# Kernel tuning notes

Measured on AMD Instinct MI355X. Metric: run time of the kernel, lower is better.

Reference implementation:

```python
import jax, jax.numpy as jnp
import numpy as np

N, E, DIN, DH, HEADS, DOUT = 50000, 800000, 128, 32, 4, 16
NL_HID = 2  # num_layers - 1
HID = HEADS * DH


def setup_inputs() -> dict:
    key = jax.random.key(0)
    ks = jax.random.split(key, 16)

    def w(k, shape, fan_in):
        return jax.random.normal(k, shape, jnp.float32) * (1.0 / np.sqrt(fan_in))

    return {
        "x": jax.random.normal(ks[0], (N, DIN), jnp.float32),
        "edge_index": jax.random.randint(ks[1], (2, E), 0, N, dtype=jnp.int64),
        "edge_attr": jax.random.normal(ks[2], (E, 1), jnp.float32),
        # conv1: dim_in -> (heads, dim_h)
        "W1": w(ks[3], (DIN, HID), DIN),
        "as1": w(ks[4], (HEADS, DH), DH),
        "ad1": w(ks[5], (HEADS, DH), DH),
        "b1": jnp.zeros((HID,), jnp.float32),
        # hidden convs: hid -> (heads, dim_h), stacked over NL_HID layers
        "Wh": w(ks[6], (NL_HID, HID, HID), HID),
        "ash": w(ks[7], (NL_HID, HEADS, DH), DH),
        "adh": w(ks[8], (NL_HID, HEADS, DH), DH),
        "bh": jnp.zeros((NL_HID, HID), jnp.float32),
        # conv2: hid -> (1, dim_out)
        "W2": w(ks[9], (HID, DOUT), HID),
        "as2": w(ks[10], (1, DOUT), DOUT),
        "ad2": w(ks[11], (1, DOUT), DOUT),
        "b2": jnp.zeros((DOUT,), jnp.float32),
    }


def _gat_conv(x, src, dst, W, a_s, a_d, b):
    """PyG GATConv (eval mode: attention dropout inactive), concat heads."""
    H, C = a_s.shape
    n = x.shape[0]
    h = (x @ W).reshape(n, H, C)                       # [N,H,C]
    al_s = jnp.einsum('nhc,hc->nh', h, a_s)            # [N,H]
    al_d = jnp.einsum('nhc,hc->nh', h, a_d)
    e = jax.nn.leaky_relu(al_s[src] + al_d[dst], 0.2)  # [Et,H]
    # scatter-softmax over incoming edges of each destination node
    m = jax.ops.segment_max(e, dst, num_segments=n)
    ee = jnp.exp(e - m[dst])
    denom = jax.ops.segment_sum(ee, dst, num_segments=n)
    alpha = ee / (denom[dst] + 1e-16)                  # [Et,H]
    out = jax.ops.segment_sum(h[src] * alpha[:, :, None], dst, num_segments=n)
    return out.reshape(n, H * C) + b


def reference(x, edge_index, edge_attr, W1, as1, ad1, b1, Wh, ash, adh, bh, W2, as2, ad2, b2):
    n = x.shape[0]
    # GATConv adds self-loops by default
    loops = jnp.arange(n, dtype=edge_index.dtype)
    src = jnp.concatenate([edge_index[0], loops])
    dst = jnp.concatenate([edge_index[1], loops])
    h = jax.nn.elu(_gat_conv(x, src, dst, W1, as1, ad1, b1))
    for i in range(Wh.shape[0]):  # dropout p=0.5 inactive in eval mode
        h = jax.nn.elu(_gat_conv(h, src, dst, Wh[i], ash[i], adh[i], bh[i]))
    return _gat_conv(h, src, dst, W2, as2, ad2, b2)  # heads=1 -> [N, DOUT]
```

## Files before the change

kernel.cpp:

```cpp
#include <hip/hip_runtime.h>
#include <hip/hip_bf16.h>
#include <hip/hip_fp16.h>


typedef _Float16 half8_t __attribute__((ext_vector_type(8)));
typedef float f32x4_t  __attribute__((ext_vector_type(4)));

static inline int divup(int a, int b){ return (a + b - 1) / b; }


__global__ __launch_bounds__(256) void zero_cnt_kernel(int* __restrict__ cnt, int n){
    int i = blockIdx.x * 256 + threadIdx.x;
    int4 z = {0, 0, 0, 0};
    if (i * 4 + 3 < n){
        *(int4*)(cnt + i * 4) = z;
    } else {
        for (int j = i * 4; j < n; ++j) cnt[j] = 0;
    }
}


__global__ __launch_bounds__(256) void fill_sliced_kernel(const int* __restrict__ src,
                                                          const int* __restrict__ dst,
                                                          int* __restrict__ cnt,
                                                          unsigned short* __restrict__ csr,
                                                          int E, int Et){
    int slice = blockIdx.x & 7;
    int e = (blockIdx.x >> 3) * 256 + threadIdx.x;
    if (e >= Et) return;
    int d = (e < E) ? dst[e] : (e - E);
    if ((d & 7) != slice) return;
    int s = (e < E) ? src[e] : d;
    int pos = atomicAdd(&cnt[d], 1);
    csr[(d << 6) + pos] = (unsigned short)s;
}


__global__ __launch_bounds__(256) void prep_kernel(const float* __restrict__ W1,
                                                   const float* __restrict__ Wh,
                                                   const float* __restrict__ as1,
                                                   const float* __restrict__ ad1,
                                                   const float* __restrict__ ash,
                                                   const float* __restrict__ adh,
                                                   _Float16* __restrict__ WTx){
    int id = blockIdx.x * 256 + threadIdx.x;
    if (id >= 3 * 144 * 128) return;
    int l = id / (144 * 128), rem = id % (144 * 128);
    int c = rem >> 7, k = rem & 127;
    const float* W = (l == 0) ? W1 : (Wh + (size_t)(l - 1) * 16384);
    float v = 0.f;
    if (c < 128){
        v = W[k * 128 + c];
    } else if (c < 136){
        int h = (c - 128) & 3;
        const float* a = (c < 132) ? ((l == 0) ? as1 : ash + (size_t)(l - 1) * 128)
                                   : ((l == 0) ? ad1 : adh + (size_t)(l - 1) * 128);
        const float* wr = W + k * 128 + h * 32;
        const float* ar = a + h * 32;
        float sum = 0.f;
        #pragma unroll
        for (int c2 = 0; c2 < 32; ++c2) sum += wr[c2] * ar[c2];
        v = sum;
    }
    WTx[id] = (_Float16)v;
}


template<bool F32IN>
__device__ __forceinline__ void gemm128L_body(const void* __restrict__ Xv,
                                              const _Float16* __restrict__ WTx,
                                              _Float16* __restrict__ H16,
                                              float* __restrict__ als,
                                              float* __restrict__ ald, int n){
    int wav = threadIdx.x >> 6, lane = threadIdx.x & 63;
    int nb = blockIdx.x * 16;
    int r = lane & 15, kg = lane >> 4;
    int anode = nb + r; if (anode >= n) anode = n - 1;

    half8_t a0, a1, a2, a3;
    if (F32IN){
        const float* xrow = (const float*)Xv + (size_t)anode * 128 + kg * 8;
        #pragma unroll
        for (int q = 0; q < 4; ++q){
            float4 u = *(const float4*)(xrow + q * 32);
            float4 w = *(const float4*)(xrow + q * 32 + 4);
            half8_t o = {(_Float16)u.x,(_Float16)u.y,(_Float16)u.z,(_Float16)u.w,
                         (_Float16)w.x,(_Float16)w.y,(_Float16)w.z,(_Float16)w.w};
            if (q == 0) a0 = o; else if (q == 1) a1 = o; else if (q == 2) a2 = o; else a3 = o;
        }
    } else {
        const _Float16* xrow = (const _Float16*)Xv + (size_t)anode * 128 + kg * 8;
        a0 = *(const half8_t*)(xrow);
        a1 = *(const half8_t*)(xrow + 32);
        a2 = *(const half8_t*)(xrow + 64);
        a3 = *(const half8_t*)(xrow + 96);
    }

    const _Float16* wc0 = WTx + (size_t)(wav * 32 + r) * 128 + kg * 8;
    const _Float16* wc1 = wc0 + 16 * 128;

    f32x4_t c0 = {0.f,0.f,0.f,0.f}, c1 = {0.f,0.f,0.f,0.f};
    c0 = __builtin_amdgcn_mfma_f32_16x16x32_f16(a0, *(const half8_t*)(wc0     ), c0, 0,0,0);
    c1 = __builtin_amdgcn_mfma_f32_16x16x32_f16(a0, *(const half8_t*)(wc1     ), c1, 0,0,0);
    c0 = __builtin_amdgcn_mfma_f32_16x16x32_f16(a1, *(const half8_t*)(wc0 + 32), c0, 0,0,0);
    c1 = __builtin_amdgcn_mfma_f32_16x16x32_f16(a1, *(const half8_t*)(wc1 + 32), c1, 0,0,0);
    c0 = __builtin_amdgcn_mfma_f32_16x16x32_f16(a2, *(const half8_t*)(wc0 + 64), c0, 0,0,0);
    c1 = __builtin_amdgcn_mfma_f32_16x16x32_f16(a2, *(const half8_t*)(wc1 + 64), c1, 0,0,0);
    c0 = __builtin_amdgcn_mfma_f32_16x16x32_f16(a3, *(const half8_t*)(wc0 + 96), c0, 0,0,0);
    c1 = __builtin_amdgcn_mfma_f32_16x16x32_f16(a3, *(const half8_t*)(wc1 + 96), c1, 0,0,0);

    int colw = wav * 32 + r;
    #pragma unroll
    for (int rg = 0; rg < 4; ++rg){
        int onode = nb + kg * 4 + rg;
        if (onode < n){
            _Float16* hr = H16 + (size_t)onode * 128 + colw;
            hr[0]  = (_Float16)c0[rg];
            hr[16] = (_Float16)c1[rg];
        }
    }

    if (wav == 0){
        const _Float16* wl = WTx + (size_t)(128 + r) * 128 + kg * 8;
        f32x4_t cl = {0.f,0.f,0.f,0.f};
        cl = __builtin_amdgcn_mfma_f32_16x16x32_f16(a0, *(const half8_t*)(wl     ), cl, 0,0,0);
        cl = __builtin_amdgcn_mfma_f32_16x16x32_f16(a1, *(const half8_t*)(wl + 32), cl, 0,0,0);
        cl = __builtin_amdgcn_mfma_f32_16x16x32_f16(a2, *(const half8_t*)(wl + 64), cl, 0,0,0);
        cl = __builtin_amdgcn_mfma_f32_16x16x32_f16(a3, *(const half8_t*)(wl + 96), cl, 0,0,0);
        if (r < 8){
            #pragma unroll
            for (int rg = 0; rg < 4; ++rg){
                int onode = nb + kg * 4 + rg;
                if (onode < n){
                    if (r < 4) als[(size_t)onode * 4 + r]       = cl[rg];
                    else       ald[(size_t)onode * 4 + (r - 4)] = cl[rg];
                }
            }
        }
    }
}

__global__ __launch_bounds__(256) void gemm128L_f32_kernel(const float* __restrict__ X,
                                                           const _Float16* __restrict__ WTx,
                                                           _Float16* __restrict__ H16,
                                                           float* __restrict__ als,
                                                           float* __restrict__ ald, int n){
    gemm128L_body<true>(X, WTx, H16, als, ald, n);
}

__global__ __launch_bounds__(256) void gemm128L_f16_kernel(const _Float16* __restrict__ X16,
                                                           const _Float16* __restrict__ WTx,
                                                           _Float16* __restrict__ H16,
                                                           float* __restrict__ als,
                                                           float* __restrict__ ald, int n){
    gemm128L_body<false>(X16, WTx, H16, als, ald, n);
}


__global__ __launch_bounds__(256) void aggregate128_kernel(const __half* __restrict__ H16,
                                                           const float* __restrict__ als,
                                                           const float* __restrict__ ald,
                                                           const int* __restrict__ cnt,
                                                           const unsigned short* __restrict__ csr,
                                                           const float* __restrict__ bias,
                                                           _Float16* __restrict__ out16,
                                                           int n){
    int node = blockIdx.x * 4 + (threadIdx.x >> 6);
    int lane = threadIdx.x & 63;
    if (node >= n) return;
    int start = node << 6, end = start + cnt[node];

    int eg = lane >> 4, cl = lane & 15;
    int h = cl >> 2;
    float ad_h = ald[(size_t)node * 4 + h];

    float den = 0.f;
    float acc[8] = {0,0,0,0,0,0,0,0};
    const __half* Hc = H16 + cl * 8;
    int i = start + eg;
    for (; i + 4 < end; i += 8){
        int sA = csr[i];
        int sB = csr[i + 4];
        float eA = als[(size_t)sA * 4 + h] + ad_h; eA = eA > 0.f ? eA : 0.2f * eA;
        float eB = als[(size_t)sB * 4 + h] + ad_h; eB = eB > 0.f ? eB : 0.2f * eB;
        float wA = __expf(eA);
        float wB = __expf(eB);
        den += wA + wB;
        uint4 ra = *(const uint4*)(Hc + (size_t)sA * 128);
        uint4 rb = *(const uint4*)(Hc + (size_t)sB * 128);
        float2 a0 = __half22float2(*(__half2*)&ra.x);
        float2 a1 = __half22float2(*(__half2*)&ra.y);
        float2 a2 = __half22float2(*(__half2*)&ra.z);
        float2 a3 = __half22float2(*(__half2*)&ra.w);
        float2 b0 = __half22float2(*(__half2*)&rb.x);
        float2 b1 = __half22float2(*(__half2*)&rb.y);
        float2 b2 = __half22float2(*(__half2*)&rb.z);
        float2 b3 = __half22float2(*(__half2*)&rb.w);
        acc[0] += wA * a0.x + wB * b0.x; acc[1] += wA * a0.y + wB * b0.y;
        acc[2] += wA * a1.x + wB * b1.x; acc[3] += wA * a1.y + wB * b1.y;
        acc[4] += wA * a2.x + wB * b2.x; acc[5] += wA * a2.y + wB * b2.y;
        acc[6] += wA * a3.x + wB * b3.x; acc[7] += wA * a3.y + wB * b3.y;
    }
    if (i < end){
        int s = csr[i];
        float e = als[(size_t)s * 4 + h] + ad_h; e = e > 0.f ? e : 0.2f * e;
        float w = __expf(e);
        den += w;
        uint4 ra = *(const uint4*)(Hc + (size_t)s * 128);
        float2 a0 = __half22float2(*(__half2*)&ra.x);
        float2 a1 = __half22float2(*(__half2*)&ra.y);
        float2 a2 = __half22float2(*(__half2*)&ra.z);
        float2 a3 = __half22float2(*(__half2*)&ra.w);
        acc[0] += w * a0.x; acc[1] += w * a0.y;
        acc[2] += w * a1.x; acc[3] += w * a1.y;
        acc[4] += w * a2.x; acc[5] += w * a2.y;
        acc[6] += w * a3.x; acc[7] += w * a3.y;
    }
    #pragma unroll
    for (int j = 0; j < 8; ++j){
        acc[j] += __shfl_xor(acc[j], 16);
        acc[j] += __shfl_xor(acc[j], 32);
    }
    den += __shfl_xor(den, 16);
    den += __shfl_xor(den, 32);

    if (eg == 0){
        float inv = 1.f / (den + 1e-16f);
        int col = cl * 8;
        float4 bv0 = *(const float4*)(bias + col);
        float4 bv1 = *(const float4*)(bias + col + 4);
        float v[8];
        v[0] = acc[0]*inv + bv0.x; v[1] = acc[1]*inv + bv0.y;
        v[2] = acc[2]*inv + bv0.z; v[3] = acc[3]*inv + bv0.w;
        v[4] = acc[4]*inv + bv1.x; v[5] = acc[5]*inv + bv1.y;
        v[6] = acc[6]*inv + bv1.z; v[7] = acc[7]*inv + bv1.w;
        #pragma unroll
        for (int j = 0; j < 8; ++j) v[j] = v[j] > 0.f ? v[j] : __expf(v[j]) - 1.f;

        half8_t o16 = {(_Float16)v[0], (_Float16)v[1], (_Float16)v[2], (_Float16)v[3],
                       (_Float16)v[4], (_Float16)v[5], (_Float16)v[6], (_Float16)v[7]};
        *(half8_t*)&out16[(size_t)node * 128 + col] = o16;
    }
}


__global__ __launch_bounds__(256) void gemm16_kernel(const _Float16* __restrict__ X16,
                                                     const float* __restrict__ W,
                                                     float* __restrict__ H4, int n){
    __shared__ float Ws[128 * 16];
    int tid = threadIdx.x;
    for (int i = tid; i < 2048; i += 256) Ws[i] = W[i];
    __syncthreads();
    int gid = blockIdx.x * 256 + tid;
    if (gid >= n * 16) return;
    int j = gid & 15, node = gid >> 4;
    const half8_t* xr = (const half8_t*)(X16 + (size_t)node * 128);
    float s = 0.f;
    #pragma unroll 4
    for (int k8 = 0; k8 < 16; ++k8){
        half8_t xv = xr[k8];
        #pragma unroll
        for (int t = 0; t < 8; ++t) s += (float)xv[t] * Ws[(k8 * 8 + t) * 16 + j];
    }
    H4[gid] = s;
}

__global__ __launch_bounds__(256) void al16_kernel(const float* __restrict__ H4,
                                                   const float* __restrict__ as2,
                                                   const float* __restrict__ ad2,
                                                   float* __restrict__ als4,
                                                   float* __restrict__ ald4, int n){
    int node = blockIdx.x * 256 + threadIdx.x;
    if (node >= n) return;
    const float4* hr = (const float4*)(H4 + (size_t)node * 16);
    const float4* asr = (const float4*)as2;
    const float4* adr = (const float4*)ad2;
    float ss = 0.f, sd = 0.f;
    #pragma unroll
    for (int i = 0; i < 4; ++i){
        float4 hv = hr[i], av = asr[i], dv = adr[i];
        ss += hv.x*av.x + hv.y*av.y + hv.z*av.z + hv.w*av.w;
        sd += hv.x*dv.x + hv.y*dv.y + hv.z*dv.z + hv.w*dv.w;
    }
    als4[node] = ss; ald4[node] = sd;
}


__global__ __launch_bounds__(256) void aggregate16_kernel(const float* __restrict__ H4,
                                                          const float* __restrict__ als4,
                                                          const float* __restrict__ ald4,
                                                          const int* __restrict__ cnt,
                                                          const unsigned short* __restrict__ csr,
                                                          const float* __restrict__ bias,
                                                          float* __restrict__ out, int n){
    int node = blockIdx.x * 4 + (threadIdx.x >> 6);
    int lane = threadIdx.x & 63;
    if (node >= n) return;
    int start = node << 6, end = start + cnt[node];
    float adn = ald4[node];

    int eg = lane >> 2, cl = lane & 3;
    float den = 0.f;
    float acc0 = 0.f, acc1 = 0.f, acc2 = 0.f, acc3 = 0.f;
    for (int i = start + eg; i < end; i += 16){
        int s = csr[i];
        float e = als4[s] + adn; e = e > 0.f ? e : 0.2f * e;
        float w = __expf(e);
        den += w;
        float4 hv = *(const float4*)(H4 + (size_t)s * 16 + cl * 4);
        acc0 += w * hv.x; acc1 += w * hv.y; acc2 += w * hv.z; acc3 += w * hv.w;
    }
    #pragma unroll
    for (int off = 4; off <= 32; off <<= 1){
        acc0 += __shfl_xor(acc0, off); acc1 += __shfl_xor(acc1, off);
        acc2 += __shfl_xor(acc2, off); acc3 += __shfl_xor(acc3, off);
        den  += __shfl_xor(den,  off);
    }

    if (eg == 0){
        float inv = 1.f / (den + 1e-16f);
        float4 bv = *(const float4*)(bias + cl * 4);
        float4 o = {acc0*inv + bv.x, acc1*inv + bv.y, acc2*inv + bv.z, acc3*inv + bv.w};
        *(float4*)&out[(size_t)node * 16 + cl * 4] = o;
    }
}


extern "C" void kernel_launch(void* const* d_in, const int* in_sizes, int n_in,
                              void* d_out, int out_size, void* d_ws, size_t ws_size,
                              hipStream_t stream) {
    const float* x   = (const float*)d_in[0];
    const int*   ei  = (const int*)d_in[1];
    const float* W1  = (const float*)d_in[3];
    const float* as1 = (const float*)d_in[4];
    const float* ad1 = (const float*)d_in[5];
    const float* b1  = (const float*)d_in[6];
    const float* Wh  = (const float*)d_in[7];
    const float* ash = (const float*)d_in[8];
    const float* adh = (const float*)d_in[9];
    const float* bh  = (const float*)d_in[10];
    const float* W2  = (const float*)d_in[11];
    const float* as2 = (const float*)d_in[12];
    const float* ad2 = (const float*)d_in[13];
    const float* b2  = (const float*)d_in[14];

    int N = in_sizes[0] / 128;
    int E = in_sizes[1] / 2;
    int Et = E + N;
    const int* srcA = ei;
    const int* dstA = ei + E;

    char* ws = (char*)d_ws;
    size_t off = 0;
    auto alloc = [&](size_t bytes) -> void* {
        void* p = ws + off;
        off = (off + bytes + 255) & ~(size_t)255;
        return p;
    };
    int* cnt      = (int*)alloc((size_t)N * 4);
    unsigned short* csr = (unsigned short*)alloc((size_t)N * 64 * 2);
    _Float16* xbuf16 = (_Float16*)alloc((size_t)N * 128 * 2);
    _Float16* h16    = (_Float16*)alloc((size_t)N * 128 * 2);
    _Float16* wtx    = (_Float16*)alloc((size_t)3 * 144 * 128 * 2);
    float* als_a  = (float*)alloc((size_t)N * 4 * 4);
    float* ald_a  = (float*)alloc((size_t)N * 4 * 4);
    float* h4     = (float*)alloc((size_t)N * 16 * 4);
    float* als4   = (float*)alloc((size_t)N * 4);
    float* ald4   = (float*)alloc((size_t)N * 4);

    zero_cnt_kernel<<<divup(divup(N, 4), 256), 256, 0, stream>>>(cnt, N);
    prep_kernel<<<divup(3 * 144 * 128, 256), 256, 0, stream>>>(W1, Wh, as1, ad1, ash, adh, wtx);
    fill_sliced_kernel<<<divup(Et, 256) * 8, 256, 0, stream>>>(srcA, dstA, cnt, csr, E, Et);

    float* out = (float*)d_out;
    const size_t WSTRIDE = (size_t)144 * 128;

    gemm128L_f32_kernel<<<divup(N, 16), 256, 0, stream>>>(x, wtx, h16, als_a, ald_a, N);
    aggregate128_kernel<<<divup(N, 4), 256, 0, stream>>>((const __half*)h16, als_a, ald_a, cnt, csr,
                                                        b1, xbuf16, N);
    gemm128L_f16_kernel<<<divup(N, 16), 256, 0, stream>>>(xbuf16, wtx + WSTRIDE, h16, als_a, ald_a, N);
    aggregate128_kernel<<<divup(N, 4), 256, 0, stream>>>((const __half*)h16, als_a, ald_a, cnt, csr,
                                                        bh, xbuf16, N);
    gemm128L_f16_kernel<<<divup(N, 16), 256, 0, stream>>>(xbuf16, wtx + 2 * WSTRIDE, h16, als_a, ald_a, N);
    aggregate128_kernel<<<divup(N, 4), 256, 0, stream>>>((const __half*)h16, als_a, ald_a, cnt, csr,
                                                        bh + 128, xbuf16, N);

    gemm16_kernel<<<divup(N * 16, 256), 256, 0, stream>>>(xbuf16, W2, h4, N);
    al16_kernel<<<divup(N, 256), 256, 0, stream>>>(h4, as2, ad2, als4, ald4, N);
    aggregate16_kernel<<<divup(N, 4), 256, 0, stream>>>(h4, als4, ald4, cnt, csr, b2, out, N);
}
```

Baseline: 266.5 us.

## Fuse final-layer GEMM and attention logits into one MFMA kernel with fp16 features

Replaces the scalar final-layer GEMM and the separate attention-logit kernel with one MFMA kernel. It uses a precomputed fp16 weight matrix whose extra columns hold W2·as2 and W2·ad2, so the logits come out of the same matrix multiply. The final hidden features are stored as fp16 instead of fp32, which halves gather traffic in the last aggregation. The CSR fill slicing also now uses bits 4-6 of the destination instead of the low bits, changing which blocks contend on atomics. The cost is fp16 rounding of the final-layer features and the folded logit weights.

```diff
diff --git a/kernel.cpp b/kernel.cpp
--- a/kernel.cpp
+++ b/kernel.cpp
@@ -29,7 +29,7 @@
     int e = (blockIdx.x >> 3) * 256 + threadIdx.x;
     if (e >= Et) return;
     int d = (e < E) ? dst[e] : (e - E);
-    if ((d & 7) != slice) return;
+    if (((d >> 4) & 7) != slice) return;
     int s = (e < E) ? src[e] : d;
     int pos = atomicAdd(&cnt[d], 1);
     csr[(d << 6) + pos] = (unsigned short)s;
@@ -42,27 +42,47 @@
                                                    const float* __restrict__ ad1,
                                                    const float* __restrict__ ash,
                                                    const float* __restrict__ adh,
-                                                   _Float16* __restrict__ WTx){
+                                                   const float* __restrict__ W2,
+                                                   const float* __restrict__ as2,
+                                                   const float* __restrict__ ad2,
+                                                   _Float16* __restrict__ WTx,
+                                                   _Float16* __restrict__ W2x){
     int id = blockIdx.x * 256 + threadIdx.x;
-    if (id >= 3 * 144 * 128) return;
-    int l = id / (144 * 128), rem = id % (144 * 128);
-    int c = rem >> 7, k = rem & 127;
-    const float* W = (l == 0) ? W1 : (Wh + (size_t)(l - 1) * 16384);
-    float v = 0.f;
-    if (c < 128){
-        v = W[k * 128 + c];
-    } else if (c < 136){
-        int h = (c - 128) & 3;
-        const float* a = (c < 132) ? ((l == 0) ? as1 : ash + (size_t)(l - 1) * 128)
-                                   : ((l == 0) ? ad1 : adh + (size_t)(l - 1) * 128);
-        const float* wr = W + k * 128 + h * 32;
-        const float* ar = a + h * 32;
-        float sum = 0.f;
-        #pragma unroll
-        for (int c2 = 0; c2 < 32; ++c2) sum += wr[c2] * ar[c2];
-        v = sum;
-    }
-    WTx[id] = (_Float16)v;
+    const int MAIN = 3 * 144 * 128;
+    if (id < MAIN){
+        int l = id / (144 * 128), rem = id % (144 * 128);
+        int c = rem >> 7, k = rem & 127;
+        const float* W = (l == 0) ? W1 : (Wh + (size_t)(l - 1) * 16384);
+        float v = 0.f;
+        if (c < 128){
+            v = W[k * 128 + c];
+        } else if (c < 136){
+            int h = (c - 128) & 3;
+            const float* a = (c < 132) ? ((l == 0) ? as1 : ash + (size_t)(l - 1) * 128)
+                                       : ((l == 0) ? ad1 : adh + (size_t)(l - 1) * 128);
+            const float* wr = W + k * 128 + h * 32;
+            const float* ar = a + h * 32;
+            float sum = 0.f;
+            #pragma unroll
+            for (int c2 = 0; c2 < 32; ++c2) sum += wr[c2] * ar[c2];
+            v = sum;
+        }
+        WTx[id] = (_Float16)v;
+    } else if (id < MAIN + 32 * 128){
+        int id2 = id - MAIN;
+        int c = id2 >> 7, k = id2 & 127;
+        float v = 0.f;
+        if (c < 16){
+            v = W2[k * 16 + c];
+        } else if (c == 16 || c == 17){
+            const float* a = (c == 16) ? as2 : ad2;
+            float sum = 0.f;
+            #pragma unroll
+            for (int j = 0; j < 16; ++j) sum += W2[k * 16 + j] * a[j];
+            v = sum;
+        }
+        W2x[id2] = (_Float16)v;
+    }
 }
 
 
@@ -154,6 +174,47 @@
                                                            float* __restrict__ als,
                                                            float* __restrict__ ald, int n){
     gemm128L_body<false>(X16, WTx, H16, als, ald, n);
+}
+
+
+__global__ __launch_bounds__(256) void gemm16L_kernel(const _Float16* __restrict__ X16,
+                                                      const _Float16* __restrict__ W2x,
+                                                      _Float16* __restrict__ H4,
+                                                      float* __restrict__ als4,
+                                                      float* __restrict__ ald4, int n){
+    int wav = threadIdx.x >> 6, lane = threadIdx.x & 63;
+    int nb = blockIdx.x * 64 + wav * 16;
+    int r = lane & 15, kg = lane >> 4;
+    int anode = nb + r; if (anode >= n) anode = n - 1;
+
+    const _Float16* xrow = X16 + (size_t)anode * 128 + kg * 8;
+    half8_t a0 = *(const half8_t*)(xrow);
+    half8_t a1 = *(const half8_t*)(xrow + 32);
+    half8_t a2 = *(const half8_t*)(xrow + 64);
+    half8_t a3 = *(const half8_t*)(xrow + 96);
+
+    const _Float16* wc0 = W2x + (size_t)r * 128 + kg * 8;
+    const _Float16* wc1 = wc0 + 16 * 128;
+
+    f32x4_t c0 = {0.f,0.f,0.f,0.f}, c1 = {0.f,0.f,0.f,0.f};
+    c0 = __builtin_amdgcn_mfma_f32_16x16x32_f16(a0, *(const half8_t*)(wc0     ), c0, 0,0,0);
+    c1 = __builtin_amdgcn_mfma_f32_16x16x32_f16(a0, *(const half8_t*)(wc1     ), c1, 0,0,0);
+    c0 = __builtin_amdgcn_mfma_f32_16x16x32_f16(a1, *(const half8_t*)(wc0 + 32), c0, 0,0,0);
+    c1 = __builtin_amdgcn_mfma_f32_16x16x32_f16(a1, *(const half8_t*)(wc1 + 32), c1, 0,0,0);
+    c0 = __builtin_amdgcn_mfma_f32_16x16x32_f16(a2, *(const half8_t*)(wc0 + 64), c0, 0,0,0);
+    c1 = __builtin_amdgcn_mfma_f32_16x16x32_f16(a2, *(const half8_t*)(wc1 + 64), c1, 0,0,0);
+    c0 = __builtin_amdgcn_mfma_f32_16x16x32_f16(a3, *(const half8_t*)(wc0 + 96), c0, 0,0,0);
+    c1 = __builtin_amdgcn_mfma_f32_16x16x32_f16(a3, *(const half8_t*)(wc1 + 96), c1, 0,0,0);
+
+    #pragma unroll
+    for (int rg = 0; rg < 4; ++rg){
+        int onode = nb + kg * 4 + rg;
+        if (onode < n){
+            H4[(size_t)onode * 16 + r] = (_Float16)c0[rg];
+            if (r == 0) als4[onode] = c1[rg];
+            else if (r == 1) ald4[onode] = c1[rg];
+        }
+    }
 }
 
 
@@ -244,49 +305,7 @@
 }
 
 
-__global__ __launch_bounds__(256) void gemm16_kernel(const _Float16* __restrict__ X16,
-                                                     const float* __restrict__ W,
-                                                     float* __restrict__ H4, int n){
-    __shared__ float Ws[128 * 16];
-    int tid = threadIdx.x;
-    for (int i = tid; i < 2048; i += 256) Ws[i] = W[i];
-    __syncthreads();
-    int gid = blockIdx.x * 256 + tid;
-    if (gid >= n * 16) return;
-    int j = gid & 15, node = gid >> 4;
-    const half8_t* xr = (const half8_t*)(X16 + (size_t)node * 128);
-    float s = 0.f;
-    #pragma unroll 4
-    for (int k8 = 0; k8 < 16; ++k8){
-        half8_t xv = xr[k8];
-        #pragma unroll
-        for (int t = 0; t < 8; ++t) s += (float)xv[t] * Ws[(k8 * 8 + t) * 16 + j];
-    }
-    H4[gid] = s;
-}
-
-__global__ __launch_bounds__(256) void al16_kernel(const float* __restrict__ H4,
-                                                   const float* __restrict__ as2,
-                                                   const float* __restrict__ ad2,
-                                                   float* __restrict__ als4,
-                                                   float* __restrict__ ald4, int n){
-    int node = blockIdx.x * 256 + threadIdx.x;
-    if (node >= n) return;
-    const float4* hr = (const float4*)(H4 + (size_t)node * 16);
-    const float4* asr = (const float4*)as2;
-    const float4* adr = (const float4*)ad2;
-    float ss = 0.f, sd = 0.f;
-    #pragma unroll
-    for (int i = 0; i < 4; ++i){
-        float4 hv = hr[i], av = asr[i], dv = adr[i];
-        ss += hv.x*av.x + hv.y*av.y + hv.z*av.z + hv.w*av.w;
-        sd += hv.x*dv.x + hv.y*dv.y + hv.z*dv.z + hv.w*dv.w;
-    }
-    als4[node] = ss; ald4[node] = sd;
-}
-
-
-__global__ __launch_bounds__(256) void aggregate16_kernel(const float* __restrict__ H4,
+__global__ __launch_bounds__(256) void aggregate16_kernel(const _Float16* __restrict__ H4,
                                                           const float* __restrict__ als4,
                                                           const float* __restrict__ ald4,
                                                           const int* __restrict__ cnt,
@@ -307,8 +326,10 @@
         float e = als4[s] + adn; e = e > 0.f ? e : 0.2f * e;
         float w = __expf(e);
         den += w;
-        float4 hv = *(const float4*)(H4 + (size_t)s * 16 + cl * 4);
-        acc0 += w * hv.x; acc1 += w * hv.y; acc2 += w * hv.z; acc3 += w * hv.w;
+        uint2 hv = *(const uint2*)(H4 + (size_t)s * 16 + cl * 4);
+        float2 h0 = __half22float2(*(__half2*)&hv.x);
+        float2 h1 = __half22float2(*(__half2*)&hv.y);
+        acc0 += w * h0.x; acc1 += w * h0.y; acc2 += w * h1.x; acc3 += w * h1.y;
     }
     #pragma unroll
     for (int off = 4; off <= 32; off <<= 1){
@@ -362,14 +383,16 @@
     _Float16* xbuf16 = (_Float16*)alloc((size_t)N * 128 * 2);
     _Float16* h16    = (_Float16*)alloc((size_t)N * 128 * 2);
     _Float16* wtx    = (_Float16*)alloc((size_t)3 * 144 * 128 * 2);
+    _Float16* w2x    = (_Float16*)alloc((size_t)32 * 128 * 2);
     float* als_a  = (float*)alloc((size_t)N * 4 * 4);
     float* ald_a  = (float*)alloc((size_t)N * 4 * 4);
-    float* h4     = (float*)alloc((size_t)N * 16 * 4);
+    _Float16* h4  = (_Float16*)alloc((size_t)N * 16 * 2);
     float* als4   = (float*)alloc((size_t)N * 4);
     float* ald4   = (float*)alloc((size_t)N * 4);
 
     zero_cnt_kernel<<<divup(divup(N, 4), 256), 256, 0, stream>>>(cnt, N);
-    prep_kernel<<<divup(3 * 144 * 128, 256), 256, 0, stream>>>(W1, Wh, as1, ad1, ash, adh, wtx);
+    prep_kernel<<<divup(3 * 144 * 128 + 32 * 128, 256), 256, 0, stream>>>(
+        W1, Wh, as1, ad1, ash, adh, W2, as2, ad2, wtx, w2x);
     fill_sliced_kernel<<<divup(Et, 256) * 8, 256, 0, stream>>>(srcA, dstA, cnt, csr, E, Et);
 
     float* out = (float*)d_out;
@@ -385,7 +408,6 @@
     aggregate128_kernel<<<divup(N, 4), 256, 0, stream>>>((const __half*)h16, als_a, ald_a, cnt, csr,
                                                         bh + 128, xbuf16, N);
 
-    gemm16_kernel<<<divup(N * 16, 256), 256, 0, stream>>>(xbuf16, W2, h4, N);
-    al16_kernel<<<divup(N, 256), 256, 0, stream>>>(h4, as2, ad2, als4, ald4, N);
+    gemm16L_kernel<<<divup(N, 64), 256, 0, stream>>>(xbuf16, w2x, h4, als4, ald4, N);
     aggregate16_kernel<<<divup(N, 4), 256, 0, stream>>>(h4, als4, ald4, cnt, csr, b2, out, N);
 }
```

New measurement: 259.0 us. -2.8%, faster.
